# Kernel optimization log

Measured on AMD Instinct MI355X. Metric: run time of the kernel, lower is better.

Reference implementation:

```python
import jax, jax.numpy as jnp
import numpy as np

EMBED_DIM = 1024
NUM_HEADS = 16
HEAD_DIM = EMBED_DIM // NUM_HEADS
TOPK_INIT = 0.3  # learnable scalar in torch; k = int(S*sigmoid(topk)) is non-differentiable, so static here


def setup_inputs() -> dict:
    rng = jax.random.key(0)
    ks = jax.random.split(rng, 11)
    L, N, E = 2048, 2, EMBED_DIM
    S = 2048
    w = 1.0 / np.sqrt(E)
    return {
        "query": jax.random.normal(ks[0], (L, N, E), jnp.float32),
        "key": jax.random.normal(ks[1], (S, N, E), jnp.float32),
        "value": jax.random.normal(ks[2], (S, N, E), jnp.float32),
        "Wq": jax.random.normal(ks[3], (E, E), jnp.float32) * w,
        "bq": jax.random.normal(ks[4], (E,), jnp.float32) * 0.02,
        "Wk": jax.random.normal(ks[5], (E, E), jnp.float32) * w,
        "bk": jax.random.normal(ks[6], (E,), jnp.float32) * 0.02,
        "Wv": jax.random.normal(ks[7], (E, E), jnp.float32) * w,
        "bv": jax.random.normal(ks[8], (E,), jnp.float32) * 0.02,
        "Wo": jax.random.normal(ks[9], (E, E), jnp.float32) * w,
        "bo": jax.random.normal(ks[10], (E,), jnp.float32) * 0.02,
    }


def reference(query, key, value, Wq, bq, Wk, bk, Wv, bv, Wo, bo):
    L, N, E = query.shape
    S = key.shape[0]
    H, D = NUM_HEADS, HEAD_DIM

    # Linear projections (nn.Linear: y = x @ W.T + b), then [L/S,N,E] -> [N,L/S,H,D]
    q = (query @ Wq.T + bq).reshape(L, N, H, D).transpose(1, 0, 2, 3)
    k = (key @ Wk.T + bk).reshape(S, N, H, D).transpose(1, 0, 2, 3)
    v = (value @ Wv.T + bv).reshape(S, N, H, D).transpose(1, 0, 2, 3)

    # [N, L, H, S]
    scores = jnp.einsum('nlhd,nshd->nlhs', q, k) / np.sqrt(D).astype(np.float32)

    # per-query top-k sparsification; k is static (int() of sigmoid(param) in torch)
    k_sel = int(S * (1.0 / (1.0 + np.exp(-TOPK_INIT))))
    _, topk_idx = jax.lax.top_k(scores, k_sel)
    keep = jnp.put_along_axis(
        jnp.zeros(scores.shape, dtype=bool), topk_idx, True, axis=-1, inplace=False
    )
    scores = jnp.where(keep, scores, -jnp.inf)
    attn = jax.nn.softmax(scores, axis=-1)

    # [N, L, D, H] (note d-major, h-minor ordering matches torch's view(L,N,E))
    out = jnp.einsum('nlhs,nshd->nldh', attn, v)
    out = out.transpose(1, 0, 2, 3).reshape(L, N, E)
    return out @ Wo.T + bo
```

## Files before the change

kernel.cpp:

```cpp
#include <hip/hip_runtime.h>
#include <hip/hip_bf16.h>
#include <hip/hip_fp16.h>


#define KSEL 1176u
#define SROW 2048
#define HSTR 132

typedef __attribute__((ext_vector_type(8))) short bf16x8;
typedef __attribute__((ext_vector_type(8))) _Float16 f16x8;
typedef __attribute__((ext_vector_type(4))) float f32x4;
typedef unsigned short ushort_t;

union S8 { bf16x8 v; ushort_t u[8]; };
union H8 { f16x8 v; ushort_t u[8]; };

#define MFMA16(A, B, C)  __builtin_amdgcn_mfma_f32_16x16x32_bf16(A, B, C, 0, 0, 0)
#define MFMAH16(A, B, C) __builtin_amdgcn_mfma_f32_16x16x32_f16(A, B, C, 0, 0, 0)

__device__ __forceinline__ ushort_t f2bf(float x) {
  unsigned u = __float_as_uint(x);
  return (ushort_t)((u + 0x7FFFu + ((u >> 16) & 1u)) >> 16);
}
__device__ __forceinline__ float bf2f(ushort_t b) {
  return __uint_as_float(((unsigned)b) << 16);
}
__device__ __forceinline__ ushort_t f2h(float x) {
  return __half_as_ushort(__float2half(x));
}
__device__ __forceinline__ float h2f(ushort_t b) {
  return __half2float(__ushort_as_half(b));
}

__device__ __forceinline__ void cvt8(ushort_t* dst, float4 p, float4 q) {
  H8 t;
  t.u[0] = f2h(p.x); t.u[1] = f2h(p.y); t.u[2] = f2h(p.z); t.u[3] = f2h(p.w);
  t.u[4] = f2h(q.x); t.u[5] = f2h(q.y); t.u[6] = f2h(q.z); t.u[7] = f2h(q.w);
  *(f16x8*)dst = t.v;
}

__global__ __launch_bounds__(256) void presplit_w(
    const float* __restrict__ W0, const float* __restrict__ W1,
    const float* __restrict__ W2, const float* __restrict__ W3,
    ushort_t* __restrict__ Whi, ushort_t* __restrict__ Wlo) {
  const int m = blockIdx.y;
  const float* W = (m == 0) ? W0 : (m == 1) ? W1 : (m == 2) ? W2 : W3;
  const size_t off = ((size_t)blockIdx.x * 256 + threadIdx.x) * 8;
  const size_t base = (size_t)m * 1048576 + off;
  if (m == 3) {
    const int f = (int)(off >> 10);
    const int r = (int)(off & 1023);
    const int hcol = r >> 6, d0 = r & 63;
    S8 hi_, lo_;
#pragma unroll
    for (int j = 0; j < 8; j++) {
      float x = W[(size_t)f * 1024 + (size_t)(d0 + j) * 16 + hcol];
      ushort_t hb = f2bf(x);
      hi_.u[j] = hb;
      lo_.u[j] = f2bf(x - bf2f(hb));
    }
    *(bf16x8*)&Whi[base] = hi_.v;
    *(bf16x8*)&Wlo[base] = lo_.v;
  } else {
    float4 p = *(const float4*)&W[off];
    float4 q = *(const float4*)&W[off + 4];
    cvt8(&Whi[base], p, q);
  }
}

__global__ __launch_bounds__(256, 4) void proj_qkv(
    const float* __restrict__ Xq, const float* __restrict__ Xk,
    const float* __restrict__ Xv, const float* __restrict__ bq,
    const float* __restrict__ bk, const float* __restrict__ bv,
    const ushort_t* __restrict__ Whi, ushort_t* __restrict__ Qf,
    ushort_t* __restrict__ Kf, ushort_t* __restrict__ Vt) {
  __shared__ ushort_t Ah[64 * 72], Bh[128 * 72];
  const int z = blockIdx.z;
  const float* X = (z == 0) ? Xq : (z == 1) ? Xk : Xv;
  const float* bias = (z == 0) ? bq : (z == 1) ? bk : bv;
  const size_t zoff = (size_t)z * 1048576;

  const int tid = threadIdx.x;
  const int n0 = blockIdx.x * 128, m0 = blockIdx.y * 64;
  const int lane = tid & 63, wv = tid >> 6;
  const int lg = lane >> 4, lq = lane & 15;
  const int wr = wv >> 1, wc = wv & 1;
  const int sr = tid >> 2, c8 = (tid & 3) * 8;

  f32x4 acc[2][4] = {};

  const float* Xr = &X[(size_t)(m0 + sr) * 1024 + c8];
  const ushort_t* Bg0 = Whi + zoff + (size_t)(n0 + sr) * 1024 + c8;
  const ushort_t* Bg1 = Bg0 + 64 * 1024;

  float4 a0 = *(const float4*)&Xr[0],  a1 = *(const float4*)&Xr[4];
  float4 a2 = *(const float4*)&Xr[32], a3 = *(const float4*)&Xr[36];
  f16x8 pb0 = *(const f16x8*)&Bg0[0], pb1 = *(const f16x8*)&Bg0[32];
  f16x8 pb2 = *(const f16x8*)&Bg1[0], pb3 = *(const f16x8*)&Bg1[32];

  for (int k0 = 0; k0 < 1024; k0 += 64) {
    __syncthreads();
    cvt8(&Ah[sr * 72 + c8], a0, a1);
    cvt8(&Ah[sr * 72 + c8 + 32], a2, a3);
    *(f16x8*)&Bh[sr * 72 + c8] = pb0;
    *(f16x8*)&Bh[sr * 72 + c8 + 32] = pb1;
    *(f16x8*)&Bh[(64 + sr) * 72 + c8] = pb2;
    *(f16x8*)&Bh[(64 + sr) * 72 + c8 + 32] = pb3;
    if (k0 + 64 < 1024) {
      const float* Xn = Xr + k0 + 64;
      a0 = *(const float4*)&Xn[0];  a1 = *(const float4*)&Xn[4];
      a2 = *(const float4*)&Xn[32]; a3 = *(const float4*)&Xn[36];
      pb0 = *(const f16x8*)&Bg0[k0 + 64];
      pb1 = *(const f16x8*)&Bg0[k0 + 96];
      pb2 = *(const f16x8*)&Bg1[k0 + 64];
      pb3 = *(const f16x8*)&Bg1[k0 + 96];
    }
    __syncthreads();
#pragma unroll
    for (int kh = 0; kh < 2; kh++) {
      const int ko = kh * 32 + lg * 8;
      f16x8 bh0 = *(const f16x8*)&Bh[(wc * 64 + lq) * 72 + ko];
      f16x8 bh1 = *(const f16x8*)&Bh[(wc * 64 + 16 + lq) * 72 + ko];
      f16x8 bh2 = *(const f16x8*)&Bh[(wc * 64 + 32 + lq) * 72 + ko];
      f16x8 bh3 = *(const f16x8*)&Bh[(wc * 64 + 48 + lq) * 72 + ko];
#pragma unroll
      for (int i = 0; i < 2; i++) {
        f16x8 ahv = *(const f16x8*)&Ah[(wr * 32 + i * 16 + lq) * 72 + ko];
        acc[i][0] = MFMAH16(ahv, bh0, acc[i][0]);
        acc[i][1] = MFMAH16(ahv, bh1, acc[i][1]);
        acc[i][2] = MFMAH16(ahv, bh2, acc[i][2]);
        acc[i][3] = MFMAH16(ahv, bh3, acc[i][3]);
      }
    }
  }

  ushort_t* dqk = (z == 0) ? Qf : Kf;
#pragma unroll
  for (int i = 0; i < 2; i++)
#pragma unroll
    for (int j = 0; j < 4; j++)
#pragma unroll
      for (int ri = 0; ri < 4; ri++) {
        int m = m0 + wr * 32 + i * 16 + 4 * lg + ri;
        int e = n0 + wc * 64 + j * 16 + lq;
        float v = acc[i][j][ri] + bias[e];
        int l = m >> 1, n = m & 1, hh = e >> 6, d = e & 63;
        if (z == 2) {
          Vt[((size_t)(n * 16 + hh) * 64 + d) * 2048 + l] = f2h(v);
        } else {
          float x = (z == 0) ? v * (0.125f * 1.4426950408889634f) : v;
          dqk[((size_t)(n * 16 + hh) * 2048 + l) * 64 + d] = f2h(x);
        }
      }
}

__global__ __launch_bounds__(256, 4) void proj_out(
    const ushort_t* __restrict__ AOhi, const ushort_t* __restrict__ AOlo,
    const ushort_t* __restrict__ Whi3, const ushort_t* __restrict__ Wlo3,
    const float* __restrict__ bias, float* __restrict__ out) {
  __shared__ ushort_t Ah[64 * 72], Al[64 * 72], Bh[64 * 72], Bl[64 * 72];
  const int tid = threadIdx.x;
  const int n0 = blockIdx.x * 64, m0 = blockIdx.y * 64;
  const int lane = tid & 63, wv = tid >> 6;
  const int lg = lane >> 4, lq = lane & 15;
  const int wr = wv >> 1, wc = wv & 1;
  const int sr = tid >> 2, c8 = (tid & 3) * 8;

  f32x4 acc[2][2] = {};

  const size_t abase = (size_t)(m0 + sr) * 64 + c8;
  const ushort_t* Bhg = Whi3 + (size_t)(n0 + sr) * 1024 + c8;
  const ushort_t* Blg = Wlo3 + (size_t)(n0 + sr) * 1024 + c8;

  bf16x8 pa0 = *(const bf16x8*)&AOhi[abase], pa1 = *(const bf16x8*)&AOhi[abase + 32];
  bf16x8 pc0 = *(const bf16x8*)&AOlo[abase], pc1 = *(const bf16x8*)&AOlo[abase + 32];
  bf16x8 pb0 = *(const bf16x8*)&Bhg[0], pb1 = *(const bf16x8*)&Bhg[32];
  bf16x8 pl0 = *(const bf16x8*)&Blg[0], pl1 = *(const bf16x8*)&Blg[32];

  for (int k0 = 0; k0 < 1024; k0 += 64) {
    __syncthreads();
    *(bf16x8*)&Ah[sr * 72 + c8] = pa0;  *(bf16x8*)&Ah[sr * 72 + c8 + 32] = pa1;
    *(bf16x8*)&Al[sr * 72 + c8] = pc0;  *(bf16x8*)&Al[sr * 72 + c8 + 32] = pc1;
    *(bf16x8*)&Bh[sr * 72 + c8] = pb0;  *(bf16x8*)&Bh[sr * 72 + c8 + 32] = pb1;
    *(bf16x8*)&Bl[sr * 72 + c8] = pl0;  *(bf16x8*)&Bl[sr * 72 + c8 + 32] = pl1;
    if (k0 + 64 < 1024) {
      const size_t an = abase + (size_t)((k0 >> 6) + 1) * 262144;
      pa0 = *(const bf16x8*)&AOhi[an]; pa1 = *(const bf16x8*)&AOhi[an + 32];
      pc0 = *(const bf16x8*)&AOlo[an]; pc1 = *(const bf16x8*)&AOlo[an + 32];
      pb0 = *(const bf16x8*)&Bhg[k0 + 64]; pb1 = *(const bf16x8*)&Bhg[k0 + 96];
      pl0 = *(const bf16x8*)&Blg[k0 + 64]; pl1 = *(const bf16x8*)&Blg[k0 + 96];
    }
    __syncthreads();
#pragma unroll
    for (int kh = 0; kh < 2; kh++) {
      const int ko = kh * 32 + lg * 8;
      bf16x8 bh0 = *(const bf16x8*)&Bh[(wc * 32 + lq) * 72 + ko];
      bf16x8 bh1 = *(const bf16x8*)&Bh[(wc * 32 + 16 + lq) * 72 + ko];
      bf16x8 bl0 = *(const bf16x8*)&Bl[(wc * 32 + lq) * 72 + ko];
      bf16x8 bl1 = *(const bf16x8*)&Bl[(wc * 32 + 16 + lq) * 72 + ko];
#pragma unroll
      for (int i = 0; i < 2; i++) {
        bf16x8 ahv = *(const bf16x8*)&Ah[(wr * 32 + i * 16 + lq) * 72 + ko];
        bf16x8 alv = *(const bf16x8*)&Al[(wr * 32 + i * 16 + lq) * 72 + ko];
        acc[i][0] = MFMA16(ahv, bh0, acc[i][0]);
        acc[i][0] = MFMA16(alv, bh0, acc[i][0]);
        acc[i][0] = MFMA16(ahv, bl0, acc[i][0]);
        acc[i][1] = MFMA16(ahv, bh1, acc[i][1]);
        acc[i][1] = MFMA16(alv, bh1, acc[i][1]);
        acc[i][1] = MFMA16(ahv, bl1, acc[i][1]);
      }
    }
  }

#pragma unroll
  for (int i = 0; i < 2; i++)
#pragma unroll
    for (int j = 0; j < 2; j++)
#pragma unroll
      for (int ri = 0; ri < 4; ri++) {
        int m = m0 + wr * 32 + i * 16 + 4 * lg + ri;
        int e = n0 + wc * 32 + j * 16 + lq;
        out[(size_t)m * 1024 + e] = acc[i][j][ri] + bias[e];
      }
}

template <bool RANKMAP>
__device__ __forceinline__ void scan_row(const unsigned* hrow, unsigned target,
                                         int lane, int* binOut, unsigned* remOut) {
  unsigned c0, c1, c2, c3;
  if (RANKMAP) {
    const bool neg = lane >= 32;
    const int ho = neg ? (lane << 1) : (62 - (lane << 1));
    uint2 hw = *(const uint2*)&hrow[ho];
    unsigned a0 = hw.x & 0xffffu, a1 = hw.x >> 16;
    unsigned a2 = hw.y & 0xffffu, a3 = hw.y >> 16;
    c0 = neg ? a0 : a3; c1 = neg ? a1 : a2;
    c2 = neg ? a2 : a1; c3 = neg ? a3 : a0;
  } else {
    uint2 hw = *(const uint2*)&hrow[lane << 1];
    c0 = hw.x & 0xffffu; c1 = hw.x >> 16;
    c2 = hw.y & 0xffffu; c3 = hw.y >> 16;
  }
  unsigned s4 = c0 + c1 + c2 + c3, incl = s4;
#pragma unroll
  for (int off = 1; off < 64; off <<= 1) {
    unsigned t = __shfl_up(incl, off);
    if (lane >= off) incl += t;
  }
  unsigned excl = incl - s4;
  bool found = (excl < target) && (target <= incl);
  int b = 0; unsigned rm = 1;
  if (found) {
    unsigned cum = excl;
    if (cum + c0 >= target) { b = (lane << 2); rm = target - cum; }
    else { cum += c0;
      if (cum + c1 >= target) { b = (lane << 2) + 1; rm = target - cum; }
      else { cum += c1;
        if (cum + c2 >= target) { b = (lane << 2) + 2; rm = target - cum; }
        else { cum += c2; b = (lane << 2) + 3; rm = target - cum; } } }
  }
  unsigned long long bal = __ballot(found);
  int src = (int)__builtin_ctzll(bal);
  *binOut = __shfl(b, src);
  *remOut = (unsigned)__shfl((int)rm, src);
}

#define KLOAD(F, gg)                                                   \
  do {                                                                 \
    _Pragma("unroll") for (int tt = 0; tt < 4; tt++) {                 \
      const int koff = ((gg) * 4 + tt) * 1024;                         \
      F[tt * 2 + 0] = *(const f16x8*)&kbase[koff];                     \
      F[tt * 2 + 1] = *(const f16x8*)&kbase[koff + 32];                \
    }                                                                  \
  } while (0)

#define KCOMP(F, gg)                                                          \
  do {                                                                        \
    _Pragma("unroll") for (int tt = 0; tt < 4; tt++) {                        \
      f32x4 acc_ = {0.f, 0.f, 0.f, 0.f};                                      \
      acc_ = MFMAH16(F[tt * 2 + 0], qf0, acc_);                               \
      acc_ = MFMAH16(F[tt * 2 + 1], qf1, acc_);                               \
      uint2 pw_;                                                              \
      pw_.x = (unsigned)f2h(acc_[0]) | ((unsigned)f2h(acc_[1]) << 16);        \
      pw_.y = (unsigned)f2h(acc_[2]) | ((unsigned)f2h(acc_[3]) << 16);        \
      atomicAdd(&histP[lq * HSTR + ((pw_.x >> 9) & 0x7Fu)],                   \
                1u << (((pw_.x >> 8) & 1u) << 4));                            \
      atomicAdd(&histP[lq * HSTR + (pw_.x >> 25)],                            \
                1u << (((pw_.x >> 24) & 1u) << 4));                           \
      atomicAdd(&histP[lq * HSTR + ((pw_.y >> 9) & 0x7Fu)],                   \
                1u << (((pw_.y >> 8) & 1u) << 4));                            \
      atomicAdd(&histP[lq * HSTR + (pw_.y >> 25)],                            \
                1u << (((pw_.y >> 24) & 1u) << 4));                           \
      const int st_ = (w * 16 + (gg) * 4 + tt) * 16;                          \
      *(uint2*)&scH[lq * SROW + ((st_ + 4 * lg) ^ xr8q)] = pw_;               \
    }                                                                         \
  } while (0)

__global__ __launch_bounds__(512, 2) void sparse_attn(
    const ushort_t* __restrict__ Qf, const ushort_t* __restrict__ Kfp,
    const ushort_t* __restrict__ Vt, ushort_t* __restrict__ AOhi,
    ushort_t* __restrict__ AOlo) {
  __shared__ ushort_t scH[16 * SROW];
  __shared__ unsigned histP[16 * HSTR];
  __shared__ float Obuf[16 * 68];
  __shared__ float dinvS[16];

  const int flat = blockIdx.x + 128 * (blockIdx.y + 16 * blockIdx.z);
  const int idx = (flat & 7) * 512 + (flat >> 3);
  const int lb = idx & 127, h = (idx >> 7) & 15, n = idx >> 11;

  const int tid = threadIdx.x;
  const int lane = tid & 63, w = tid >> 6;
  const int lg = lane >> 4, lq = lane & 15;
  const int xr8q = (lq & 7) << 3;
  const size_t nh = (size_t)(n * 16 + h);

  for (int i = tid; i < 16 * HSTR; i += 512) histP[i] = 0u;
  for (int i = tid; i < 16 * 68; i += 512) Obuf[i] = 0.f;

  const size_t qo = (nh * 2048 + (size_t)lb * 16 + lq) * 64 + lg * 8;
  const f16x8 qf0 = *(const f16x8*)&Qf[qo];
  const f16x8 qf1 = *(const f16x8*)&Qf[qo + 32];

  const ushort_t* Kf = Kfp + nh * 2048 * 64;
  const ushort_t* kbase = Kf + (size_t)(w * 256 + lq) * 64 + lg * 8;

  __syncthreads();

  {
    f16x8 fa[8], fb[8];
    KLOAD(fa, 0);
    for (int g = 0; g < 4; g += 2) {
      KLOAD(fb, g + 1);
      KCOMP(fa, g);
      if (g + 2 < 4) KLOAD(fa, g + 2);
      KCOMP(fb, g + 1);
    }
  }
  __syncthreads();

  for (int rr = 0; rr < 2; rr++) {
    const int r = w * 2 + rr;
    const int rb = r * SROW;
    const int xr = (r & 7) << 3;
    unsigned* hrow = &histP[r * HSTR];

    int b1r; unsigned rem;
    scan_row<true>(hrow, KSEL, lane, &b1r, &rem);
    const unsigned rb1 = (b1r < 128) ? (unsigned)(b1r ^ 0x7F) : (unsigned)b1r;
    const unsigned sxor = (rb1 & 0x80u) ? 0u : 0xFFu;

    uint4 rv0 = *(const uint4*)&scH[rb + ((0 * 512 + lane * 8) ^ xr)];
    uint4 rv1 = *(const uint4*)&scH[rb + ((1 * 512 + lane * 8) ^ xr)];
    uint4 rv2 = *(const uint4*)&scH[rb + ((2 * 512 + lane * 8) ^ xr)];
    uint4 rv3 = *(const uint4*)&scH[rb + ((3 * 512 + lane * 8) ^ xr)];

    *(uint2*)&hrow[lane << 1] = make_uint2(0u, 0u);
    __threadfence_block();
    auto refine1 = [&](unsigned wd) {
      if (((wd >> 8) & 0xFFu) == rb1) {
        unsigned sr_ = (wd & 0xFFu) ^ sxor;
        atomicAdd(&hrow[sr_ >> 1], 1u << ((sr_ & 1u) << 4));
      }
      if ((wd >> 24) == rb1) {
        unsigned sr_ = ((wd >> 16) & 0xFFu) ^ sxor;
        atomicAdd(&hrow[sr_ >> 1], 1u << ((sr_ & 1u) << 4));
      }
    };
    refine1(rv0.x); refine1(rv0.y); refine1(rv0.z); refine1(rv0.w);
    refine1(rv1.x); refine1(rv1.y); refine1(rv1.z); refine1(rv1.w);
    refine1(rv2.x); refine1(rv2.y); refine1(rv2.z); refine1(rv2.w);
    refine1(rv3.x); refine1(rv3.y); refine1(rv3.z); refine1(rv3.w);
    __threadfence_block();
    int b2r; unsigned rem2;
    scan_row<false>(hrow, rem, lane, &b2r, &rem2);
    (void)rem2;
    const unsigned vbits = (rb1 << 8) | (((unsigned)b2r) ^ sxor);
    const float fV = h2f((ushort_t)vbits);

    float den = 0.f;
    auto exp2w = [&](unsigned wd) -> unsigned {
      float f0 = h2f((ushort_t)(wd & 0xffffu));
      float f1 = h2f((ushort_t)(wd >> 16));
      float e0 = (f0 >= fV) ? __builtin_amdgcn_exp2f(f0) : 0.f;
      float e1 = (f1 >= fV) ? __builtin_amdgcn_exp2f(f1) : 0.f;
      den += e0 + e1;
      return (unsigned)f2h(e0) | ((unsigned)f2h(e1) << 16);
    };
    uint4 ov;
    ov.x = exp2w(rv0.x); ov.y = exp2w(rv0.y); ov.z = exp2w(rv0.z); ov.w = exp2w(rv0.w);
    *(uint4*)&scH[rb + ((0 * 512 + lane * 8) ^ xr)] = ov;
    ov.x = exp2w(rv1.x); ov.y = exp2w(rv1.y); ov.z = exp2w(rv1.z); ov.w = exp2w(rv1.w);
    *(uint4*)&scH[rb + ((1 * 512 + lane * 8) ^ xr)] = ov;
    ov.x = exp2w(rv2.x); ov.y = exp2w(rv2.y); ov.z = exp2w(rv2.z); ov.w = exp2w(rv2.w);
    *(uint4*)&scH[rb + ((2 * 512 + lane * 8) ^ xr)] = ov;
    ov.x = exp2w(rv3.x); ov.y = exp2w(rv3.y); ov.z = exp2w(rv3.z); ov.w = exp2w(rv3.w);
    *(uint4*)&scH[rb + ((3 * 512 + lane * 8) ^ xr)] = ov;

#pragma unroll
    for (int off = 32; off > 0; off >>= 1) den += __shfl_xor(den, off);
    if (lane == 0) dinvS[r] = 1.0f / den;
  }
  __syncthreads();

  {
    const int db = w & 3, sh = w >> 2;
    const int sOff = sh * 1024;
    const ushort_t* Vb =
        Vt + (nh * 64 + (size_t)(db * 16 + lq)) * 2048 + sOff;
    const int xw = (lq & 7) << 3;
    const int arow = lq * SROW;
    f32x4 o0 = {0.f, 0.f, 0.f, 0.f}, o1 = o0, o2 = o0, o3 = o0;
    f16x8 va0 = *(const f16x8*)&Vb[lg * 8];
    f16x8 va1 = *(const f16x8*)&Vb[32 + lg * 8];
    f16x8 vb0 = *(const f16x8*)&Vb[64 + lg * 8];
    f16x8 vb1 = *(const f16x8*)&Vb[96 + lg * 8];
#pragma unroll 2
    for (int c = 0; c < 16; c += 2) {
      f16x8 na0, na1, nb0, nb1;
      if (c + 2 < 16) {
        na0 = *(const f16x8*)&Vb[(c + 2) * 64 + lg * 8];
        na1 = *(const f16x8*)&Vb[(c + 2) * 64 + 32 + lg * 8];
        nb0 = *(const f16x8*)&Vb[(c + 3) * 64 + lg * 8];
        nb1 = *(const f16x8*)&Vb[(c + 3) * 64 + 32 + lg * 8];
      }
      f16x8 pa0 = *(const f16x8*)&scH[arow + ((sOff + c * 64 + lg * 8) ^ xw)];
      f16x8 pa1 = *(const f16x8*)&scH[arow + ((sOff + c * 64 + 32 + lg * 8) ^ xw)];
      o0 = MFMAH16(pa0, va0, o0);
      o1 = MFMAH16(pa1, va1, o1);
      f16x8 pb0_ = *(const f16x8*)&scH[arow + ((sOff + (c + 1) * 64 + lg * 8) ^ xw)];
      f16x8 pb1_ = *(const f16x8*)&scH[arow + ((sOff + (c + 1) * 64 + 32 + lg * 8) ^ xw)];
      o2 = MFMAH16(pb0_, vb0, o2);
      o3 = MFMAH16(pb1_, vb1, o3);
      va0 = na0; va1 = na1; vb0 = nb0; vb1 = nb1;
    }
    f32x4 oa = (o0 + o1) + (o2 + o3);
#pragma unroll
    for (int ri = 0; ri < 4; ri++) {
      int q = lg * 4 + ri;
      atomicAdd(&Obuf[q * 68 + db * 16 + lq], oa[ri]);
    }
  }
  __syncthreads();

  {
#pragma unroll
    for (int rep = 0; rep < 2; rep++) {
      int idx2 = tid + rep * 512;
      int q = idx2 >> 6, d = idx2 & 63;
      float val = Obuf[q * 68 + d] * dinvS[q];
      size_t ai = ((size_t)h * 4096 + (size_t)(lb * 16 + q) * 2 + n) * 64 +
                  (size_t)d;
      ushort_t hb = f2bf(val);
      AOhi[ai] = hb;
      AOlo[ai] = f2bf(val - bf2f(hb));
    }
  }
}

extern "C" void kernel_launch(void* const* d_in, const int* in_sizes, int n_in,
                              void* d_out, int out_size, void* d_ws, size_t ws_size,
                              hipStream_t stream) {
  const float* query = (const float*)d_in[0];
  const float* key   = (const float*)d_in[1];
  const float* value = (const float*)d_in[2];
  const float* Wq    = (const float*)d_in[3];
  const float* bq    = (const float*)d_in[4];
  const float* Wk    = (const float*)d_in[5];
  const float* bk    = (const float*)d_in[6];
  const float* Wv    = (const float*)d_in[7];
  const float* bv    = (const float*)d_in[8];
  const float* Wo    = (const float*)d_in[9];
  const float* bo    = (const float*)d_in[10];

  ushort_t* Qf   = (ushort_t*)d_ws;
  ushort_t* Kf   = Qf + 4194304;
  ushort_t* Vt   = Kf + 4194304;
  ushort_t* AOhi = Vt + 4194304;
  ushort_t* AOlo = AOhi + 4194304;
  ushort_t* Whi  = AOlo + 4194304;
  ushort_t* Wlo  = Whi + 4194304;

  dim3 block(256);
  presplit_w<<<dim3(512, 4), block, 0, stream>>>(Wq, Wk, Wv, Wo, Whi, Wlo);

  proj_qkv<<<dim3(8, 64, 3), block, 0, stream>>>(query, key, value, bq, bk, bv,
                                                 Whi, Qf, Kf, Vt);

  sparse_attn<<<dim3(128, 16, 2), dim3(512), 0, stream>>>(Qf, Kf, Vt, AOhi, AOlo);

  proj_out<<<dim3(16, 64), block, 0, stream>>>(AOhi, AOlo, Whi + 3 * 1048576,
                                               Wlo + 3 * 1048576, bo,
                                               (float*)d_out);
}
```

Baseline: 357.3 us.

## Interleave two-row top-k selection, prefetch K/V early, raise occupancy bound

Processes both softmax/top-k rows per warp together instead of sequentially, interleaving their histogram refinement and exp passes to expose more independent LDS and ALU work. The first K tile load is issued before the initial barrier, and the first V fragments are loaded before the selection phase so global latency overlaps with the selection work. Launch bounds change from 2 to 4 blocks per CU, which forces tighter register allocation. LDS use per block (about 70KB) likely prevents 4 blocks from fitting anyway, so the occupancy hint may only cause spills, and holding the extra row and prefetch registers adds pressure.

```diff
diff --git a/kernel.cpp b/kernel.cpp
--- a/kernel.cpp
+++ b/kernel.cpp
@@ -296,7 +296,7 @@
     }                                                                         \
   } while (0)
 
-__global__ __launch_bounds__(512, 2) void sparse_attn(
+__global__ __launch_bounds__(512, 4) void sparse_attn(
     const ushort_t* __restrict__ Qf, const ushort_t* __restrict__ Kfp,
     const ushort_t* __restrict__ Vt, ushort_t* __restrict__ AOhi,
     ushort_t* __restrict__ AOlo) {
@@ -325,11 +325,12 @@
   const ushort_t* Kf = Kfp + nh * 2048 * 64;
   const ushort_t* kbase = Kf + (size_t)(w * 256 + lq) * 64 + lg * 8;
 
+  f16x8 fa[8], fb[8];
+  KLOAD(fa, 0);
+
   __syncthreads();
 
   {
-    f16x8 fa[8], fb[8];
-    KLOAD(fa, 0);
     for (int g = 0; g < 4; g += 2) {
       KLOAD(fb, g + 1);
       KCOMP(fa, g);
@@ -339,82 +340,128 @@
   }
   __syncthreads();
 
-  for (int rr = 0; rr < 2; rr++) {
-    const int r = w * 2 + rr;
-    const int rb = r * SROW;
-    const int xr = (r & 7) << 3;
-    unsigned* hrow = &histP[r * HSTR];
-
-    int b1r; unsigned rem;
-    scan_row<true>(hrow, KSEL, lane, &b1r, &rem);
-    const unsigned rb1 = (b1r < 128) ? (unsigned)(b1r ^ 0x7F) : (unsigned)b1r;
-    const unsigned sxor = (rb1 & 0x80u) ? 0u : 0xFFu;
-
-    uint4 rv0 = *(const uint4*)&scH[rb + ((0 * 512 + lane * 8) ^ xr)];
-    uint4 rv1 = *(const uint4*)&scH[rb + ((1 * 512 + lane * 8) ^ xr)];
-    uint4 rv2 = *(const uint4*)&scH[rb + ((2 * 512 + lane * 8) ^ xr)];
-    uint4 rv3 = *(const uint4*)&scH[rb + ((3 * 512 + lane * 8) ^ xr)];
-
-    *(uint2*)&hrow[lane << 1] = make_uint2(0u, 0u);
+  const int db3 = w & 3, sh3 = w >> 2;
+  const int sOff3 = sh3 * 1024;
+  const ushort_t* Vb = Vt + (nh * 64 + (size_t)(db3 * 16 + lq)) * 2048 + sOff3;
+  f16x8 pv0 = *(const f16x8*)&Vb[lg * 8];
+  f16x8 pv1 = *(const f16x8*)&Vb[32 + lg * 8];
+  f16x8 pv2 = *(const f16x8*)&Vb[64 + lg * 8];
+  f16x8 pv3 = *(const f16x8*)&Vb[96 + lg * 8];
+
+  {
+    const int r0 = w * 2, r1 = r0 + 1;
+    const int ba = r0 * SROW, bb = r1 * SROW;
+    const int xa = (r0 & 7) << 3, xb = (r1 & 7) << 3;
+    unsigned* hrow0 = &histP[r0 * HSTR];
+    unsigned* hrow1 = &histP[r1 * HSTR];
+
+    uint4 rA0 = *(const uint4*)&scH[ba + ((0 * 512 + lane * 8) ^ xa)];
+    uint4 rA1 = *(const uint4*)&scH[ba + ((1 * 512 + lane * 8) ^ xa)];
+    uint4 rA2 = *(const uint4*)&scH[ba + ((2 * 512 + lane * 8) ^ xa)];
+    uint4 rA3 = *(const uint4*)&scH[ba + ((3 * 512 + lane * 8) ^ xa)];
+    uint4 rB0 = *(const uint4*)&scH[bb + ((0 * 512 + lane * 8) ^ xb)];
+    uint4 rB1 = *(const uint4*)&scH[bb + ((1 * 512 + lane * 8) ^ xb)];
+    uint4 rB2 = *(const uint4*)&scH[bb + ((2 * 512 + lane * 8) ^ xb)];
+    uint4 rB3 = *(const uint4*)&scH[bb + ((3 * 512 + lane * 8) ^ xb)];
+
+    int b1a, b1b; unsigned rema, remb;
+    scan_row<true>(hrow0, KSEL, lane, &b1a, &rema);
+    scan_row<true>(hrow1, KSEL, lane, &b1b, &remb);
+    const unsigned rba = (b1a < 128) ? (unsigned)(b1a ^ 0x7F) : (unsigned)b1a;
+    const unsigned sxa = (rba & 0x80u) ? 0u : 0xFFu;
+    const unsigned rbb = (b1b < 128) ? (unsigned)(b1b ^ 0x7F) : (unsigned)b1b;
+    const unsigned sxb = (rbb & 0x80u) ? 0u : 0xFFu;
+
+    *(uint2*)&hrow0[lane << 1] = make_uint2(0u, 0u);
+    *(uint2*)&hrow1[lane << 1] = make_uint2(0u, 0u);
     __threadfence_block();
-    auto refine1 = [&](unsigned wd) {
-      if (((wd >> 8) & 0xFFu) == rb1) {
-        unsigned sr_ = (wd & 0xFFu) ^ sxor;
-        atomicAdd(&hrow[sr_ >> 1], 1u << ((sr_ & 1u) << 4));
-      }
-      if ((wd >> 24) == rb1) {
-        unsigned sr_ = ((wd >> 16) & 0xFFu) ^ sxor;
-        atomicAdd(&hrow[sr_ >> 1], 1u << ((sr_ & 1u) << 4));
+
+    auto refine = [&](unsigned wd, unsigned rbx, unsigned sxx, unsigned* hr) {
+      if (((wd >> 8) & 0xFFu) == rbx) {
+        unsigned s_ = (wd & 0xFFu) ^ sxx;
+        atomicAdd(&hr[s_ >> 1], 1u << ((s_ & 1u) << 4));
+      }
+      if ((wd >> 24) == rbx) {
+        unsigned s_ = ((wd >> 16) & 0xFFu) ^ sxx;
+        atomicAdd(&hr[s_ >> 1], 1u << ((s_ & 1u) << 4));
       }
     };
-    refine1(rv0.x); refine1(rv0.y); refine1(rv0.z); refine1(rv0.w);
-    refine1(rv1.x); refine1(rv1.y); refine1(rv1.z); refine1(rv1.w);
-    refine1(rv2.x); refine1(rv2.y); refine1(rv2.z); refine1(rv2.w);
-    refine1(rv3.x); refine1(rv3.y); refine1(rv3.z); refine1(rv3.w);
+    refine(rA0.x, rba, sxa, hrow0); refine(rB0.x, rbb, sxb, hrow1);
+    refine(rA0.y, rba, sxa, hrow0); refine(rB0.y, rbb, sxb, hrow1);
+    refine(rA0.z, rba, sxa, hrow0); refine(rB0.z, rbb, sxb, hrow1);
+    refine(rA0.w, rba, sxa, hrow0); refine(rB0.w, rbb, sxb, hrow1);
+    refine(rA1.x, rba, sxa, hrow0); refine(rB1.x, rbb, sxb, hrow1);
+    refine(rA1.y, rba, sxa, hrow0); refine(rB1.y, rbb, sxb, hrow1);
+    refine(rA1.z, rba, sxa, hrow0); refine(rB1.z, rbb, sxb, hrow1);
+    refine(rA1.w, rba, sxa, hrow0); refine(rB1.w, rbb, sxb, hrow1);
+    refine(rA2.x, rba, sxa, hrow0); refine(rB2.x, rbb, sxb, hrow1);
+    refine(rA2.y, rba, sxa, hrow0); refine(rB2.y, rbb, sxb, hrow1);
+    refine(rA2.z, rba, sxa, hrow0); refine(rB2.z, rbb, sxb, hrow1);
+    refine(rA2.w, rba, sxa, hrow0); refine(rB2.w, rbb, sxb, hrow1);
+    refine(rA3.x, rba, sxa, hrow0); refine(rB3.x, rbb, sxb, hrow1);
+    refine(rA3.y, rba, sxa, hrow0); refine(rB3.y, rbb, sxb, hrow1);
+    refine(rA3.z, rba, sxa, hrow0); refine(rB3.z, rbb, sxb, hrow1);
+    refine(rA3.w, rba, sxa, hrow0); refine(rB3.w, rbb, sxb, hrow1);
     __threadfence_block();
-    int b2r; unsigned rem2;
-    scan_row<false>(hrow, rem, lane, &b2r, &rem2);
-    (void)rem2;
-    const unsigned vbits = (rb1 << 8) | (((unsigned)b2r) ^ sxor);
-    const float fV = h2f((ushort_t)vbits);
-
-    float den = 0.f;
-    auto exp2w = [&](unsigned wd) -> unsigned {
+
+    int b2a, b2b; unsigned dum;
+    scan_row<false>(hrow0, rema, lane, &b2a, &dum);
+    scan_row<false>(hrow1, remb, lane, &b2b, &dum);
+    const float fVa = h2f((ushort_t)((rba << 8) | (((unsigned)b2a) ^ sxa)));
+    const float fVb = h2f((ushort_t)((rbb << 8) | (((unsigned)b2b) ^ sxb)));
+
+    float dena = 0.f, denb = 0.f;
+    auto expw = [&](unsigned wd, float fVx, float& dn) -> unsigned {
       float f0 = h2f((ushort_t)(wd & 0xffffu));
       float f1 = h2f((ushort_t)(wd >> 16));
-      float e0 = (f0 >= fV) ? __builtin_amdgcn_exp2f(f0) : 0.f;
-      float e1 = (f1 >= fV) ? __builtin_amdgcn_exp2f(f1) : 0.f;
-      den += e0 + e1;
+      float e0 = (f0 >= fVx) ? __builtin_amdgcn_exp2f(f0) : 0.f;
+      float e1 = (f1 >= fVx) ? __builtin_amdgcn_exp2f(f1) : 0.f;
+      dn += e0 + e1;
       return (unsigned)f2h(e0) | ((unsigned)f2h(e1) << 16);
     };
-    uint4 ov;
-    ov.x = exp2w(rv0.x); ov.y = exp2w(rv0.y); ov.z = exp2w(rv0.z); ov.w = exp2w(rv0.w);
-    *(uint4*)&scH[rb + ((0 * 512 + lane * 8) ^ xr)] = ov;
-    ov.x = exp2w(rv1.x); ov.y = exp2w(rv1.y); ov.z = exp2w(rv1.z); ov.w = exp2w(rv1.w);
-    *(uint4*)&scH[rb + ((1 * 512 + lane * 8) ^ xr)] = ov;
-    ov.x = exp2w(rv2.x); ov.y = exp2w(rv2.y); ov.z = exp2w(rv2.z); ov.w = exp2w(rv2.w);
-    *(uint4*)&scH[rb + ((2 * 512 + lane * 8) ^ xr)] = ov;
-    ov.x = exp2w(rv3.x); ov.y = exp2w(rv3.y); ov.z = exp2w(rv3.z); ov.w = exp2w(rv3.w);
-    *(uint4*)&scH[rb + ((3 * 512 + lane * 8) ^ xr)] = ov;
-
-#pragma unroll
-    for (int off = 32; off > 0; off >>= 1) den += __shfl_xor(den, off);
-    if (lane == 0) dinvS[r] = 1.0f / den;
+    uint4 oa, ob;
+    oa.x = expw(rA0.x, fVa, dena); ob.x = expw(rB0.x, fVb, denb);
+    oa.y = expw(rA0.y, fVa, dena); ob.y = expw(rB0.y, fVb, denb);
+    oa.z = expw(rA0.z, fVa, dena); ob.z = expw(rB0.z, fVb, denb);
+    oa.w = expw(rA0.w, fVa, dena); ob.w = expw(rB0.w, fVb, denb);
+    *(uint4*)&scH[ba + ((0 * 512 + lane * 8) ^ xa)] = oa;
+    *(uint4*)&scH[bb + ((0 * 512 + lane * 8) ^ xb)] = ob;
+    oa.x = expw(rA1.x, fVa, dena); ob.x = expw(rB1.x, fVb, denb);
+    oa.y = expw(rA1.y, fVa, dena); ob.y = expw(rB1.y, fVb, denb);
+    oa.z = expw(rA1.z, fVa, dena); ob.z = expw(rB1.z, fVb, denb);
+    oa.w = expw(rA1.w, fVa, dena); ob.w = expw(rB1.w, fVb, denb);
+    *(uint4*)&scH[ba + ((1 * 512 + lane * 8) ^ xa)] = oa;
+    *(uint4*)&scH[bb + ((1 * 512 + lane * 8) ^ xb)] = ob;
+    oa.x = expw(rA2.x, fVa, dena); ob.x = expw(rB2.x, fVb, denb);
+    oa.y = expw(rA2.y, fVa, dena); ob.y = expw(rB2.y, fVb, denb);
+    oa.z = expw(rA2.z, fVa, dena); ob.z = expw(rB2.z, fVb, denb);
+    oa.w = expw(rA2.w, fVa, dena); ob.w = expw(rB2.w, fVb, denb);
+    *(uint4*)&scH[ba + ((2 * 512 + lane * 8) ^ xa)] = oa;
+    *(uint4*)&scH[bb + ((2 * 512 + lane * 8) ^ xb)] = ob;
+    oa.x = expw(rA3.x, fVa, dena); ob.x = expw(rB3.x, fVb, denb);
+    oa.y = expw(rA3.y, fVa, dena); ob.y = expw(rB3.y, fVb, denb);
+    oa.z = expw(rA3.z, fVa, dena); ob.z = expw(rB3.z, fVb, denb);
+    oa.w = expw(rA3.w, fVa, dena); ob.w = expw(rB3.w, fVb, denb);
+    *(uint4*)&scH[ba + ((3 * 512 + lane * 8) ^ xa)] = oa;
+    *(uint4*)&scH[bb + ((3 * 512 + lane * 8) ^ xb)] = ob;
+
+#pragma unroll
+    for (int off = 32; off > 0; off >>= 1) {
+      dena += __shfl_xor(dena, off);
+      denb += __shfl_xor(denb, off);
+    }
+    if (lane == 0) {
+      dinvS[r0] = 1.0f / dena;
+      dinvS[r1] = 1.0f / denb;
+    }
   }
   __syncthreads();
 
   {
-    const int db = w & 3, sh = w >> 2;
-    const int sOff = sh * 1024;
-    const ushort_t* Vb =
-        Vt + (nh * 64 + (size_t)(db * 16 + lq)) * 2048 + sOff;
     const int xw = (lq & 7) << 3;
     const int arow = lq * SROW;
     f32x4 o0 = {0.f, 0.f, 0.f, 0.f}, o1 = o0, o2 = o0, o3 = o0;
-    f16x8 va0 = *(const f16x8*)&Vb[lg * 8];
-    f16x8 va1 = *(const f16x8*)&Vb[32 + lg * 8];
-    f16x8 vb0 = *(const f16x8*)&Vb[64 + lg * 8];
-    f16x8 vb1 = *(const f16x8*)&Vb[96 + lg * 8];
+    f16x8 va0 = pv0, va1 = pv1, vb0 = pv2, vb1 = pv3;
 #pragma unroll 2
     for (int c = 0; c < 16; c += 2) {
       f16x8 na0, na1, nb0, nb1;
@@ -424,12 +471,12 @@
         nb0 = *(const f16x8*)&Vb[(c + 3) * 64 + lg * 8];
         nb1 = *(const f16x8*)&Vb[(c + 3) * 64 + 32 + lg * 8];
       }
-      f16x8 pa0 = *(const f16x8*)&scH[arow + ((sOff + c * 64 + lg * 8) ^ xw)];
-      f16x8 pa1 = *(const f16x8*)&scH[arow + ((sOff + c * 64 + 32 + lg * 8) ^ xw)];
+      f16x8 pa0 = *(const f16x8*)&scH[arow + ((sOff3 + c * 64 + lg * 8) ^ xw)];
+      f16x8 pa1 = *(const f16x8*)&scH[arow + ((sOff3 + c * 64 + 32 + lg * 8) ^ xw)];
       o0 = MFMAH16(pa0, va0, o0);
       o1 = MFMAH16(pa1, va1, o1);
-      f16x8 pb0_ = *(const f16x8*)&scH[arow + ((sOff + (c + 1) * 64 + lg * 8) ^ xw)];
-      f16x8 pb1_ = *(const f16x8*)&scH[arow + ((sOff + (c + 1) * 64 + 32 + lg * 8) ^ xw)];
+      f16x8 pb0_ = *(const f16x8*)&scH[arow + ((sOff3 + (c + 1) * 64 + lg * 8) ^ xw)];
+      f16x8 pb1_ = *(const f16x8*)&scH[arow + ((sOff3 + (c + 1) * 64 + 32 + lg * 8) ^ xw)];
       o2 = MFMAH16(pb0_, vb0, o2);
       o3 = MFMAH16(pb1_, vb1, o3);
       va0 = na0; va1 = na1; vb0 = nb0; vb1 = nb1;
@@ -438,7 +485,7 @@
 #pragma unroll
     for (int ri = 0; ri < 4; ri++) {
       int q = lg * 4 + ri;
-      atomicAdd(&Obuf[q * 68 + db * 16 + lq], oa[ri]);
+      atomicAdd(&Obuf[q * 68 + db3 * 16 + lq], oa[ri]);
     }
   }
   __syncthreads();
```

Result: slower. 382.7 us (+7.1%).
